# Kernel tuning notes

Measured on AMD Instinct MI355X. Metric: run time of the kernel, lower is better.

## Reference

```python
import jax, jax.numpy as jnp
import numpy as np

MIN_, MAX_, KSZ, IGNORE_IDX = 10, 10, 3, -255
B, H, W = 256, 256, 256
LI_MAX_ITERS = 64


def setup_inputs() -> dict:
    key = jax.random.key(0)
    x = jax.random.uniform(key, (B, 1, H, W), dtype=jnp.float32)
    return {"x": x}


def _otsu(hist):
    # hist: [256] counts. Returns Otsu threshold (bin value); fg = img > t.
    bins = jnp.arange(256, dtype=jnp.float32)
    w0 = jnp.cumsum(hist)[:-1]
    w1 = hist.sum() - w0
    s0 = jnp.cumsum(hist * bins)[:-1]
    s_tot = (hist * bins).sum()
    m0 = s0 / jnp.maximum(w0, 1e-12)
    m1 = (s_tot - s0) / jnp.maximum(w1, 1e-12)
    var_b = w0 * w1 * (m0 - m1) ** 2
    return jnp.argmax(var_b).astype(jnp.float32)


def _li(hist, init_t):
    # Histogram-based Li iterative minimum cross-entropy threshold
    # (skimage.filters.threshold_li with initial_guess=init_t).
    bins = jnp.arange(256, dtype=jnp.float32)
    img_min = jnp.min(jnp.where(hist > 0, bins, 255.0))
    vals = bins - img_min  # shift so values >= 0 (as skimage does)
    csum = jnp.cumsum(hist)
    cvsum = jnp.cumsum(hist * vals)
    n_tot, s_tot = csum[-1], cvsum[-1]
    tol = 0.5  # integer image -> half the minimal value spacing

    def body(state):
        t_curr, _, i = state
        # background: img <= t_curr + img_min
        idx = jnp.clip(jnp.floor(t_curr + img_min).astype(jnp.int32), 0, 255)
        n_back, s_back = csum[idx], cvsum[idx]
        n_fore, s_fore = n_tot - n_back, s_tot - s_back
        mean_back = jnp.where(n_back > 0, s_back / jnp.maximum(n_back, 1.0), 0.0)
        mean_fore = s_fore / jnp.maximum(n_fore, 1.0)
        eps = 1e-12
        t_next = (mean_back - mean_fore) / (
            jnp.log(jnp.maximum(mean_back, eps)) - jnp.log(jnp.maximum(mean_fore, eps)))
        t_next = jnp.where(mean_back < eps, mean_fore / 2.0, t_next)
        return (t_next, t_curr, i + 1)

    def cond(state):
        t_curr, t_prev, i = state
        return (jnp.abs(t_curr - t_prev) > tol) & (i < LI_MAX_ITERS)

    t0 = init_t - img_min
    t_fin, _, _ = jax.lax.while_loop(cond, body, (t0, t0 + 10.0, 0))
    return t_fin + img_min


def _sample_mask(key, region, k):
    # Uniform sampling without replacement of up to k pixels from region
    # (bool [H,W]) via random-score top-k (equiv. to torch.multinomial
    # with uniform probs, w/o replacement).
    flat = region.reshape(-1)
    scores = jnp.where(flat, jax.random.uniform(key, (flat.shape[0],)), -1.0)
    top, idx = jax.lax.top_k(scores, k)
    valid = (top >= 0.0).astype(jnp.int32)
    mask = jnp.zeros(flat.shape[0], jnp.int32).at[idx].max(valid)
    return mask.reshape(region.shape)


def _dilate(m):
    # kornia dilation with ones (KSZ,KSZ) kernel on a 0/1 mask == max filter.
    return jax.lax.reduce_window(m, 0, jax.lax.max, (KSZ, KSZ), (1, 1), "SAME")


def _per_image(img_u8, key_fg, key_bg):
    # img_u8: [H,W] int32 in [0,255]
    hist = jnp.zeros(256, jnp.float32).at[img_u8.ravel()].add(1.0)
    otsu = jnp.clip(_otsu(hist), 1.0, 254.0)  # clamp 0->1, 255->254
    li_t = _li(hist, otsu)
    roi = img_u8.astype(jnp.float32) > li_t

    fg = _sample_mask(key_fg, roi, MAX_)
    bg = _sample_mask(key_bg, jnp.logical_not(roi), MIN_)
    if KSZ > 1:
        fg = _dilate(fg)
        bg = _dilate(bg)

    overlap = (fg + bg) == 2
    fg = jnp.where(overlap, 0, fg)
    bg = jnp.where(overlap, 0, bg)

    seeds = jnp.full((H, W), IGNORE_IDX, jnp.int32)
    seeds = jnp.where(bg == 1, 0, seeds)
    seeds = jnp.where(fg == 1, 1, seeds)
    return seeds


def reference(x):
    b = x.shape[0]
    # (cam*255).astype(uint8): truncation, cam in [0,1]
    img = jnp.clip(jnp.floor(x[:, 0] * 255.0), 0, 255).astype(jnp.int32)
    keys = jax.random.split(jax.random.key(1), (b, 2))
    return jax.vmap(_per_image)(img, keys[:, 0], keys[:, 1])
```

## Files before the change

kernel.cpp:

```cpp
#include <hip/hip_runtime.h>
#include <stdint.h>

#define NPIX 65536
#define IGN (-255)
#define CAP 768
#define LCAP 192
#define HPART  16384
#define M_CF   18432
#define M_CB   18433
#define M_THR  18434
#define M_NROI 18435
#define M_FG   18436
#define M_BG   19204
#define SCR_I4 5120

__device__ __forceinline__ uint32_t rotl32(uint32_t v, uint32_t r){ return (v<<r)|(v>>(32u-r)); }

__device__ __forceinline__ void tf2x32(uint32_t k0, uint32_t k1, uint32_t x0, uint32_t x1,
                                       uint32_t &o0, uint32_t &o1){
  uint32_t k2 = k0 ^ k1 ^ 0x1BD11BDAu;
  x0 += k0; x1 += k1;
#define TFR(r) { x0 += x1; x1 = rotl32(x1,(r)); x1 ^= x0; }
  TFR(13u) TFR(15u) TFR(26u) TFR(6u)   x0 += k1; x1 += k2 + 1u;
  TFR(17u) TFR(29u) TFR(16u) TFR(24u)  x0 += k2; x1 += k0 + 2u;
  TFR(13u) TFR(15u) TFR(26u) TFR(6u)   x0 += k0; x1 += k1 + 3u;
  TFR(17u) TFR(29u) TFR(16u) TFR(24u)  x0 += k1; x1 += k2 + 4u;
  TFR(13u) TFR(15u) TFR(26u) TFR(6u)   x0 += k2; x1 += k0 + 5u;
#undef TFR
  o0 = x0; o1 = x1;
}

__device__ __forceinline__ unsigned long long packCand(uint32_t bits, uint32_t pix){
  float f = __uint_as_float((bits >> 9) | 0x3f800000u) - 1.0f;
  uint32_t u = __float_as_uint(f) ^ 0x80000000u;
  return ((unsigned long long)u << 32) | (unsigned long long)(0xFFFFFFFFu - pix);
}

__device__ __forceinline__ void t10_insert(unsigned long long* l, unsigned long long c){
  if (c > l[9]) {
    l[9] = c;
#pragma unroll
    for (int i = 9; i > 0; --i){
      unsigned long long a = l[i-1], b2 = l[i];
      if (b2 > a){ l[i-1] = b2; l[i] = a; }
    }
  }
}

__global__ __launch_bounds__(256, 8)
void k1_hist_fill(const float* __restrict__ x, int* __restrict__ out){
  const int blk = blockIdx.x;
  const int b = blk >> 3, j8 = blk & 7;
  const int tid = threadIdx.x;
  const float4* x4 = (const float4*)(x + (size_t)b * NPIX);
  int* base = out + (size_t)b * NPIX;
  int4* o4 = (int4*)base;

  __shared__ uint32_t histR[1024];
#pragma unroll
  for (int k = 0; k < 4; ++k) histR[tid + 256*k] = 0u;
  if (j8 == 0 && tid == 0){ base[M_CF] = 0; base[M_CB] = 0; }
  __syncthreads();

  const int4 f4 = make_int4(IGN, IGN, IGN, IGN);
  const uint32_t c4 = (uint32_t)(tid & 3);
#pragma unroll
  for (int jj = 0; jj < 8; ++jj){
    int i4 = j8*2048 + jj*256 + tid;
    float4 v = x4[i4];
    uint32_t u0 = (uint32_t)min(max((int)floorf(v.x*255.0f),0),255);
    uint32_t u1 = (uint32_t)min(max((int)floorf(v.y*255.0f),0),255);
    uint32_t u2 = (uint32_t)min(max((int)floorf(v.z*255.0f),0),255);
    uint32_t u3 = (uint32_t)min(max((int)floorf(v.w*255.0f),0),255);
    base[i4] = (int)(u0 | (u1<<8) | (u2<<16) | (u3<<24));
    if (i4 >= SCR_I4) o4[i4] = f4;
    atomicAdd(&histR[(u0<<2)|c4],1u); atomicAdd(&histR[(u1<<2)|c4],1u);
    atomicAdd(&histR[(u2<<2)|c4],1u); atomicAdd(&histR[(u3<<2)|c4],1u);
  }
  __syncthreads();
  uint32_t s = histR[4*tid] + histR[4*tid+1] + histR[4*tid+2] + histR[4*tid+3];
  base[HPART + j8*256 + tid] = (int)s;
}

__global__ __launch_bounds__(256, 8)
void k2_score(int* __restrict__ out){
  const int blk = blockIdx.x;
  const int b = blk >> 3, j8 = blk & 7;
  const int tid = threadIdx.x;
  int* meta = out + (size_t)b * NPIX;

  __shared__ float csum[256], cvsum[256];
  __shared__ int s_imin, s_qthr;
  __shared__ unsigned long long s_best;
  __shared__ uint32_t s_kw[4];
  __shared__ int s_lcnt[2], s_base[2];
  __shared__ int s_lbuf[2][LCAP];

  if (tid == 0){ s_imin = 255; s_best = 0ull; s_lcnt[0] = 0; s_lcnt[1] = 0; }
  if (tid < 2){
    uint32_t o0, o1;
    tf2x32(0u, 1u, 0u, (uint32_t)(2*b + tid), o0, o1);
    s_kw[2*tid] = o0; s_kw[2*tid+1] = o1;
  }
  __syncthreads();

  int h = 0;
#pragma unroll
  for (int j = 0; j < 8; ++j) h += meta[HPART + j*256 + tid];
  if (h) atomicMin(&s_imin, tid);
  __syncthreads();
  const float img_min = (float)s_imin;

  csum[tid]  = (float)h;
  cvsum[tid] = (float)h * ((float)tid - img_min);
  __syncthreads();
  for (int off = 1; off < 256; off <<= 1){
    float a = 0.f, c2 = 0.f;
    if (tid >= off){ a = csum[tid-off]; c2 = cvsum[tid-off]; }
    __syncthreads();
    if (tid >= off){ csum[tid] += a; cvsum[tid] += c2; }
    __syncthreads();
  }
  {
    float s_tot_o = cvsum[255] + img_min * csum[255];
    if (tid < 255){
      float w0 = csum[tid];
      float w1 = 65536.0f - w0;
      float cs = cvsum[tid] + img_min * csum[tid];
      float m0 = cs / fmaxf(w0, 1e-12f);
      float m1 = (s_tot_o - cs) / fmaxf(w1, 1e-12f);
      float d = m0 - m1;
      float vb = (w0*w1) * (d*d);
      unsigned long long pk =
        ((unsigned long long)__float_as_uint(vb) << 32) | (unsigned long long)(255 - tid);
      atomicMax(&s_best, pk);
    }
  }
  __syncthreads();
  if (tid == 0){
    int bestIdx = 255 - (int)(s_best & 0xFFFFFFFFull);
    float otsu = fminf(fmaxf((float)bestIdx, 1.0f), 254.0f);
    float n_tot = csum[255], s_tot = cvsum[255];
    float t_curr = otsu - img_min, t_prev = t_curr + 10.0f;
    int it = 0;
    while (fabsf(t_curr - t_prev) > 0.5f && it < 64){
      int idx = min(max((int)floorf(t_curr + img_min), 0), 255);
      float n_back = csum[idx], s_back = cvsum[idx];
      float n_fore = n_tot - n_back, s_fore = s_tot - s_back;
      float mean_back = (n_back > 0.0f) ? (s_back / fmaxf(n_back, 1.0f)) : 0.0f;
      float mean_fore = s_fore / fmaxf(n_fore, 1.0f);
      float t_next = (mean_back - mean_fore) /
                     (logf(fmaxf(mean_back, 1e-12f)) - logf(fmaxf(mean_fore, 1e-12f)));
      if (mean_back < 1e-12f) t_next = mean_fore * 0.5f;
      t_prev = t_curr; t_curr = t_next; ++it;
    }
    float lit = t_curr + img_min;
    int qthr;
    if (!(lit == lit)) qthr = 256;
    else               qthr = (int)floorf(lit) + 1;
    s_qthr = qthr;
    if (j8 == 0){
      meta[M_THR] = qthr;
      int nlo = (qthr <= 0) ? 0 : (int)csum[min(qthr, 256) - 1];
      meta[M_NROI] = NPIX - nlo;
    }
  }
  __syncthreads();

  const int qthr = s_qthr;
  const uint32_t fk0 = s_kw[0], fk1 = s_kw[1], bk0 = s_kw[2], bk1 = s_kw[3];
  const int4* u4 = (const int4*)meta;
  int4 w0 = u4[j8*512 + tid];
  int4 w1 = u4[j8*512 + 256 + tid];
  const uint32_t pixA = (uint32_t)(j8*8192 + 16*tid);
  const uint32_t pixB = pixA + 4096u;
#pragma unroll
  for (int half = 0; half < 2; ++half){
    int4 w = half ? w1 : w0;
    uint32_t pb = half ? pixB : pixA;
    const uint32_t words[4] = {(uint32_t)w.x,(uint32_t)w.y,(uint32_t)w.z,(uint32_t)w.w};
#pragma unroll
    for (int m = 0; m < 4; ++m){
      uint32_t pk = words[m];
#pragma unroll
      for (int s = 0; s < 4; ++s){
        int q = (int)((pk >> (8*s)) & 255u);
        bool r = (q >= qthr);
        uint32_t pix = pb + (uint32_t)(4*m + s);
        uint32_t o0, o1;
        tf2x32(r ? fk0 : bk0, r ? fk1 : bk1, 0u, pix, o0, o1);
        uint32_t bits = o0 ^ o1;
        if (bits >= 0xFF000000u){
          int r2 = r ? 0 : 1;
          int idx = atomicAdd(&s_lcnt[r2], 1);
          if (idx < LCAP) s_lbuf[r2][idx] = (int)pix;
        }
      }
    }
  }
  __syncthreads();
  if (tid < 2){
    int n = s_lcnt[tid];
    int add = (n > LCAP) ? (n + CAP + 1) : n;
    s_base[tid] = atomicAdd(&meta[M_CF + tid], add);
  }
  __syncthreads();
#pragma unroll
  for (int r2 = 0; r2 < 2; ++r2){
    int n = min(s_lcnt[r2], LCAP);
    int bse = s_base[r2];
    for (int i = tid; i < n; i += 256){
      int g = bse + i;
      if (g < CAP) meta[(r2 ? M_BG : M_FG) + g] = s_lbuf[r2][i];
    }
  }
}

__global__ __launch_bounds__(256, 4)
void k3_final(int* __restrict__ out){
  const int b = blockIdx.x;
  const int tid = threadIdx.x;
  int* meta = out + (size_t)b * NPIX;
  int* outb = meta;

  __shared__ unsigned long long s_top[2][64][10];
  __shared__ unsigned long long s_top2[2][8][10];
  __shared__ uint32_t s_kw[4];
  __shared__ int s_cnt[2], s_fail[2], s_np[2];
  __shared__ int s_qthr;
  __shared__ int s_pr[2][10], s_pc[2][10];

  if (tid < 2){
    uint32_t o0, o1;
    tf2x32(0u, 1u, 0u, (uint32_t)(2*b + tid), o0, o1);
    s_kw[2*tid] = o0; s_kw[2*tid+1] = o1;
  }
  if (tid == 0){
    s_qthr = meta[M_THR];
    int nroi = meta[M_NROI];
    int c0 = meta[M_CF], c1 = meta[M_CB];
    s_cnt[0] = c0; s_cnt[1] = c1;
    s_fail[0] = (c0 > CAP) || (c0 < 10 && c0 != nroi);
    s_fail[1] = (c1 > CAP) || (c1 < 10 && c1 != NPIX - nroi);
  }
  __syncthreads();

  const int wv = tid >> 6, lane = tid & 63;
  if (wv < 2){
    const int r2 = wv;
    unsigned long long t[10];
#pragma unroll
    for (int i = 0; i < 10; ++i) t[i] = 0ull;
    const uint32_t kk0 = s_kw[2*r2], kk1 = s_kw[2*r2+1];
    if (!s_fail[r2]){
      int n = min(s_cnt[r2], CAP);
      for (int i = lane; i < n; i += 64){
        uint32_t pix = (uint32_t)meta[(r2 ? M_BG : M_FG) + i];
        uint32_t o0, o1; tf2x32(kk0, kk1, 0u, pix, o0, o1);
        t10_insert(t, packCand(o0 ^ o1, pix));
      }
    } else {
      const int qthr = s_qthr;
      for (int k = 0; k < 1024; ++k){
        uint32_t pix = (uint32_t)(lane + 64*k);
        int q = (int)(((uint32_t)meta[pix >> 2] >> (8*(pix & 3u))) & 255u);
        bool r = (q >= qthr);
        if (r == (r2 == 0)){
          uint32_t o0, o1; tf2x32(kk0, kk1, 0u, pix, o0, o1);
          t10_insert(t, packCand(o0 ^ o1, pix));
        }
      }
    }
#pragma unroll
    for (int i = 0; i < 10; ++i) s_top[r2][lane][i] = t[i];
  }
  __syncthreads();
  if (wv < 2 && lane < 8){
    unsigned long long t[10];
#pragma unroll
    for (int i = 0; i < 10; ++i) t[i] = 0ull;
    for (int l2 = 0; l2 < 8; ++l2)
#pragma unroll
      for (int i = 0; i < 10; ++i) t10_insert(t, s_top[wv][lane*8 + l2][i]);
#pragma unroll
    for (int i = 0; i < 10; ++i) s_top2[wv][lane][i] = t[i];
  }
  __syncthreads();
  if (wv < 2 && lane == 0){
    unsigned long long t[10];
#pragma unroll
    for (int i = 0; i < 10; ++i) t[i] = 0ull;
    for (int l2 = 0; l2 < 8; ++l2)
#pragma unroll
      for (int i = 0; i < 10; ++i) t10_insert(t, s_top2[wv][l2][i]);
    int np = 0;
    for (int i = 0; i < 10; ++i){
      if (t[i]){
        uint32_t pix = 0xFFFFFFFFu - (uint32_t)(t[i] & 0xFFFFFFFFull);
        s_pr[wv][np] = (int)(pix >> 8);
        s_pc[wv][np] = (int)(pix & 255u);
        ++np;
      }
    }
    s_np[wv] = np;
  }
  __syncthreads();

  const int4 f4 = make_int4(IGN, IGN, IGN, IGN);
#pragma unroll
  for (int k = 0; k < 20; ++k)
    ((int4*)meta)[tid + 256*k] = f4;
  __syncthreads();

  const int nfg = s_np[0], nbg = s_np[1];
  const int npts = nfg + nbg;
  if (tid < npts*9){
    int k = tid / 9, d = tid - k*9;
    int pr = (k < nfg) ? s_pr[0][k] : s_pr[1][k - nfg];
    int pc = (k < nfg) ? s_pc[0][k] : s_pc[1][k - nfg];
    pr += d/3 - 1; pc += d%3 - 1;
    if (pr >= 0 && pr < 256 && pc >= 0 && pc < 256){
      bool fgd = false, bgd = false;
      for (int i = 0; i < nfg; ++i) fgd |= (abs(pr - s_pr[0][i]) <= 1) && (abs(pc - s_pc[0][i]) <= 1);
      for (int i = 0; i < nbg; ++i) bgd |= (abs(pr - s_pr[1][i]) <= 1) && (abs(pc - s_pc[1][i]) <= 1);
      int val = (fgd && bgd) ? IGN : (fgd ? 1 : 0);
      outb[pr*256 + pc] = val;
    }
  }
}

extern "C" void kernel_launch(void* const* d_in, const int* in_sizes, int n_in,
                              void* d_out, int out_size, void* d_ws, size_t ws_size,
                              hipStream_t stream) {
  const float* x = (const float*)d_in[0];
  int* out = (int*)d_out;
  int B = in_sizes[0] / NPIX;
  k1_hist_fill<<<8*B, 256, 0, stream>>>(x, out);
  k2_score    <<<8*B, 256, 0, stream>>>(out);
  k3_final    <<<B,   256, 0, stream>>>(out);
}
```

Measured before the change: 200.8 us.

## Prefilter random candidates for both classes in histogram pass, merge scoring into final kernel

The first kernel now runs the Threefry hash for every pixel under both the foreground and background keys while it builds the histogram. It records high-score candidates per segment, so the thresholded pixel scan of the old second kernel goes away and the packed-u8 image store is no longer needed. The final kernel computes Otsu/Li itself, re-reads the original floats only for the candidates, and builds the top-k from shared memory. This saves one launch and one full-image pass at the cost of doubling hash work in k1 and making k2 do the threshold work with only B blocks.

```diff
diff --git a/kernel.cpp b/kernel.cpp
--- a/kernel.cpp
+++ b/kernel.cpp
@@ -3,16 +3,14 @@
 
 #define NPIX 65536
 #define IGN (-255)
-#define CAP 768
-#define LCAP 192
-#define HPART  16384
-#define M_CF   18432
-#define M_CB   18433
-#define M_THR  18434
-#define M_NROI 18435
-#define M_FG   18436
-#define M_BG   19204
-#define SCR_I4 5120
+#define SEGC 96
+#define GCAP 768
+#define FGSEG 0
+#define BGSEG 768
+#define CNTF  1536
+#define CNTB  1544
+#define HPART 1552
+#define SCRI4 1024
 
 __device__ __forceinline__ uint32_t rotl32(uint32_t v, uint32_t r){ return (v<<r)|(v>>(32u-r)); }
 
@@ -48,20 +46,28 @@
 }
 
 __global__ __launch_bounds__(256, 8)
-void k1_hist_fill(const float* __restrict__ x, int* __restrict__ out){
+void k1_main(const float* __restrict__ x, int* __restrict__ out){
   const int blk = blockIdx.x;
   const int b = blk >> 3, j8 = blk & 7;
   const int tid = threadIdx.x;
   const float4* x4 = (const float4*)(x + (size_t)b * NPIX);
-  int* base = out + (size_t)b * NPIX;
-  int4* o4 = (int4*)base;
+  int* meta = out + (size_t)b * NPIX;
+  int4* o4 = (int4*)meta;
 
   __shared__ uint32_t histR[1024];
+  __shared__ uint32_t s_kw[4];
+  __shared__ int s_lcnt[2];
 #pragma unroll
   for (int k = 0; k < 4; ++k) histR[tid + 256*k] = 0u;
-  if (j8 == 0 && tid == 0){ base[M_CF] = 0; base[M_CB] = 0; }
-  __syncthreads();
-
+  if (tid < 2){
+    uint32_t o0, o1;
+    tf2x32(0u, 1u, 0u, (uint32_t)(2*b + tid), o0, o1);
+    s_kw[2*tid] = o0; s_kw[2*tid+1] = o1;
+    s_lcnt[tid] = 0;
+  }
+  __syncthreads();
+
+  const uint32_t fk0 = s_kw[0], fk1 = s_kw[1], bk0 = s_kw[2], bk1 = s_kw[3];
   const int4 f4 = make_int4(IGN, IGN, IGN, IGN);
   const uint32_t c4 = (uint32_t)(tid & 3);
 #pragma unroll
@@ -72,35 +78,56 @@
     uint32_t u1 = (uint32_t)min(max((int)floorf(v.y*255.0f),0),255);
     uint32_t u2 = (uint32_t)min(max((int)floorf(v.z*255.0f),0),255);
     uint32_t u3 = (uint32_t)min(max((int)floorf(v.w*255.0f),0),255);
-    base[i4] = (int)(u0 | (u1<<8) | (u2<<16) | (u3<<24));
-    if (i4 >= SCR_I4) o4[i4] = f4;
     atomicAdd(&histR[(u0<<2)|c4],1u); atomicAdd(&histR[(u1<<2)|c4],1u);
     atomicAdd(&histR[(u2<<2)|c4],1u); atomicAdd(&histR[(u3<<2)|c4],1u);
+    if (i4 >= SCRI4) o4[i4] = f4;
+    uint32_t pix0 = (uint32_t)(4*i4);
+#pragma unroll
+    for (int s = 0; s < 4; ++s){
+      uint32_t pix = pix0 + (uint32_t)s;
+      uint32_t a0, a1, c0, c1;
+      tf2x32(fk0, fk1, 0u, pix, a0, a1);
+      tf2x32(bk0, bk1, 0u, pix, c0, c1);
+      if ((a0 ^ a1) >= 0xFF000000u){
+        int idx = atomicAdd(&s_lcnt[0], 1);
+        if (idx < SEGC) meta[FGSEG + j8*SEGC + idx] = (int)pix;
+      }
+      if ((c0 ^ c1) >= 0xFF000000u){
+        int idx = atomicAdd(&s_lcnt[1], 1);
+        if (idx < SEGC) meta[BGSEG + j8*SEGC + idx] = (int)pix;
+      }
+    }
   }
   __syncthreads();
   uint32_t s = histR[4*tid] + histR[4*tid+1] + histR[4*tid+2] + histR[4*tid+3];
-  base[HPART + j8*256 + tid] = (int)s;
-}
-
-__global__ __launch_bounds__(256, 8)
-void k2_score(int* __restrict__ out){
-  const int blk = blockIdx.x;
-  const int b = blk >> 3, j8 = blk & 7;
+  meta[HPART + j8*256 + tid] = (int)s;
+  if (tid < 2) meta[(tid ? CNTB : CNTF) + j8] = s_lcnt[tid];
+}
+
+__global__ __launch_bounds__(256, 2)
+void k2_final(const float* __restrict__ x, int* __restrict__ out){
+  const int b = blockIdx.x;
   const int tid = threadIdx.x;
   int* meta = out + (size_t)b * NPIX;
+  int* outb = meta;
+  const float* img = x + (size_t)b * NPIX;
 
   __shared__ float csum[256], cvsum[256];
-  __shared__ int s_imin, s_qthr;
+  __shared__ int s_imin, s_qthr, s_nroi;
   __shared__ unsigned long long s_best;
   __shared__ uint32_t s_kw[4];
-  __shared__ int s_lcnt[2], s_base[2];
-  __shared__ int s_lbuf[2][LCAP];
-
-  if (tid == 0){ s_imin = 255; s_best = 0ull; s_lcnt[0] = 0; s_lcnt[1] = 0; }
+  __shared__ int s_cand[2][GCAP];
+  __shared__ int s_cc[2], s_ovf[2], s_fail[2], s_np[2];
+  __shared__ unsigned long long s_top[2][64][10];
+  __shared__ unsigned long long s_top2[2][8][10];
+  __shared__ int s_pr[2][10], s_pc[2][10];
+
+  if (tid == 0){ s_imin = 255; s_best = 0ull; }
   if (tid < 2){
     uint32_t o0, o1;
     tf2x32(0u, 1u, 0u, (uint32_t)(2*b + tid), o0, o1);
     s_kw[2*tid] = o0; s_kw[2*tid+1] = o1;
+    s_cc[tid] = 0;
   }
   __syncthreads();
 
@@ -121,6 +148,7 @@
     if (tid >= off){ csum[tid] += a; cvsum[tid] += c2; }
     __syncthreads();
   }
+
   {
     float s_tot_o = cvsum[255] + img_min * csum[255];
     if (tid < 255){
@@ -137,6 +165,7 @@
     }
   }
   __syncthreads();
+
   if (tid == 0){
     int bestIdx = 255 - (int)(s_best & 0xFFFFFFFFull);
     float otsu = fminf(fmaxf((float)bestIdx, 1.0f), 254.0f);
@@ -159,89 +188,43 @@
     if (!(lit == lit)) qthr = 256;
     else               qthr = (int)floorf(lit) + 1;
     s_qthr = qthr;
-    if (j8 == 0){
-      meta[M_THR] = qthr;
-      int nlo = (qthr <= 0) ? 0 : (int)csum[min(qthr, 256) - 1];
-      meta[M_NROI] = NPIX - nlo;
-    }
+    int nlo = (qthr <= 0) ? 0 : (int)csum[min(qthr, 256) - 1];
+    s_nroi = NPIX - nlo;
+  }
+  if (tid < 2){
+    int gc = 0, ovf = 0;
+#pragma unroll
+    for (int j = 0; j < 8; ++j){
+      int c = meta[(tid ? CNTB : CNTF) + j];
+      gc += c; if (c > SEGC) ovf = 1;
+    }
+    s_ovf[tid] = ovf | (gc > GCAP);
   }
   __syncthreads();
 
   const int qthr = s_qthr;
-  const uint32_t fk0 = s_kw[0], fk1 = s_kw[1], bk0 = s_kw[2], bk1 = s_kw[3];
-  const int4* u4 = (const int4*)meta;
-  int4 w0 = u4[j8*512 + tid];
-  int4 w1 = u4[j8*512 + 256 + tid];
-  const uint32_t pixA = (uint32_t)(j8*8192 + 16*tid);
-  const uint32_t pixB = pixA + 4096u;
-#pragma unroll
-  for (int half = 0; half < 2; ++half){
-    int4 w = half ? w1 : w0;
-    uint32_t pb = half ? pixB : pixA;
-    const uint32_t words[4] = {(uint32_t)w.x,(uint32_t)w.y,(uint32_t)w.z,(uint32_t)w.w};
-#pragma unroll
-    for (int m = 0; m < 4; ++m){
-      uint32_t pk = words[m];
-#pragma unroll
-      for (int s = 0; s < 4; ++s){
-        int q = (int)((pk >> (8*s)) & 255u);
-        bool r = (q >= qthr);
-        uint32_t pix = pb + (uint32_t)(4*m + s);
-        uint32_t o0, o1;
-        tf2x32(r ? fk0 : bk0, r ? fk1 : bk1, 0u, pix, o0, o1);
-        uint32_t bits = o0 ^ o1;
-        if (bits >= 0xFF000000u){
-          int r2 = r ? 0 : 1;
-          int idx = atomicAdd(&s_lcnt[r2], 1);
-          if (idx < LCAP) s_lbuf[r2][idx] = (int)pix;
+#pragma unroll
+  for (int r2 = 0; r2 < 2; ++r2){
+    for (int i = tid; i < GCAP; i += 256){
+      int j = i / SEGC, k = i - j*SEGC;
+      int cnt = min(meta[(r2 ? CNTB : CNTF) + j], SEGC);
+      if (k < cnt){
+        uint32_t pix = (uint32_t)meta[(r2 ? BGSEG : FGSEG) + i];
+        float v = img[pix];
+        int q = min(max((int)floorf(v*255.0f),0),255);
+        bool roi = (q >= qthr);
+        if (roi == (r2 == 0)){
+          int idx = atomicAdd(&s_cc[r2], 1);
+          s_cand[r2][idx] = (int)pix;
         }
       }
     }
   }
   __syncthreads();
   if (tid < 2){
-    int n = s_lcnt[tid];
-    int add = (n > LCAP) ? (n + CAP + 1) : n;
-    s_base[tid] = atomicAdd(&meta[M_CF + tid], add);
-  }
-  __syncthreads();
-#pragma unroll
-  for (int r2 = 0; r2 < 2; ++r2){
-    int n = min(s_lcnt[r2], LCAP);
-    int bse = s_base[r2];
-    for (int i = tid; i < n; i += 256){
-      int g = bse + i;
-      if (g < CAP) meta[(r2 ? M_BG : M_FG) + g] = s_lbuf[r2][i];
-    }
-  }
-}
-
-__global__ __launch_bounds__(256, 4)
-void k3_final(int* __restrict__ out){
-  const int b = blockIdx.x;
-  const int tid = threadIdx.x;
-  int* meta = out + (size_t)b * NPIX;
-  int* outb = meta;
-
-  __shared__ unsigned long long s_top[2][64][10];
-  __shared__ unsigned long long s_top2[2][8][10];
-  __shared__ uint32_t s_kw[4];
-  __shared__ int s_cnt[2], s_fail[2], s_np[2];
-  __shared__ int s_qthr;
-  __shared__ int s_pr[2][10], s_pc[2][10];
-
-  if (tid < 2){
-    uint32_t o0, o1;
-    tf2x32(0u, 1u, 0u, (uint32_t)(2*b + tid), o0, o1);
-    s_kw[2*tid] = o0; s_kw[2*tid+1] = o1;
-  }
-  if (tid == 0){
-    s_qthr = meta[M_THR];
-    int nroi = meta[M_NROI];
-    int c0 = meta[M_CF], c1 = meta[M_CB];
-    s_cnt[0] = c0; s_cnt[1] = c1;
-    s_fail[0] = (c0 > CAP) || (c0 < 10 && c0 != nroi);
-    s_fail[1] = (c1 > CAP) || (c1 < 10 && c1 != NPIX - nroi);
+    int rs = tid ? (NPIX - s_nroi) : s_nroi;
+    int cc = s_cc[tid];
+    s_fail[tid] = s_ovf[tid] || (cc < 10 && cc != rs);
   }
   __syncthreads();
 
@@ -253,19 +236,19 @@
     for (int i = 0; i < 10; ++i) t[i] = 0ull;
     const uint32_t kk0 = s_kw[2*r2], kk1 = s_kw[2*r2+1];
     if (!s_fail[r2]){
-      int n = min(s_cnt[r2], CAP);
+      int n = s_cc[r2];
       for (int i = lane; i < n; i += 64){
-        uint32_t pix = (uint32_t)meta[(r2 ? M_BG : M_FG) + i];
+        uint32_t pix = (uint32_t)s_cand[r2][i];
         uint32_t o0, o1; tf2x32(kk0, kk1, 0u, pix, o0, o1);
         t10_insert(t, packCand(o0 ^ o1, pix));
       }
     } else {
-      const int qthr = s_qthr;
       for (int k = 0; k < 1024; ++k){
         uint32_t pix = (uint32_t)(lane + 64*k);
-        int q = (int)(((uint32_t)meta[pix >> 2] >> (8*(pix & 3u))) & 255u);
-        bool r = (q >= qthr);
-        if (r == (r2 == 0)){
+        float v = img[pix];
+        int q = min(max((int)floorf(v*255.0f),0),255);
+        bool roi = (q >= qthr);
+        if (roi == (r2 == 0)){
           uint32_t o0, o1; tf2x32(kk0, kk1, 0u, pix, o0, o1);
           t10_insert(t, packCand(o0 ^ o1, pix));
         }
@@ -308,7 +291,7 @@
 
   const int4 f4 = make_int4(IGN, IGN, IGN, IGN);
 #pragma unroll
-  for (int k = 0; k < 20; ++k)
+  for (int k = 0; k < 4; ++k)
     ((int4*)meta)[tid + 256*k] = f4;
   __syncthreads();
 
@@ -335,7 +318,6 @@
   const float* x = (const float*)d_in[0];
   int* out = (int*)d_out;
   int B = in_sizes[0] / NPIX;
-  k1_hist_fill<<<8*B, 256, 0, stream>>>(x, out);
-  k2_score    <<<8*B, 256, 0, stream>>>(out);
-  k3_final    <<<B,   256, 0, stream>>>(out);
-}
+  k1_main <<<8*B, 256, 0, stream>>>(x, out);
+  k2_final<<<B,   256, 0, stream>>>(x, out);
+}
```

Measured after the change: 191.6 us. 1.05x faster.

## Fuse scoring and final selection into one 1024-thread per-image kernel

Applied to the files above, without the earlier changes.

Merges the per-slice scoring kernel and the final top-k/dilation kernel into a single kernel with one 1024-thread block per image. Candidates are kept as packed keys in shared memory, so the global atomics, the metadata round trip and the Threefry recomputation in the final stage go away. Otsu and Li thresholds are now computed once per image rather than eight times. The cost is less parallelism: 256 large blocks instead of 2048 small ones, plus a larger shared-memory footprint that may limit occupancy.

```diff
diff --git a/kernel.cpp b/kernel.cpp
--- a/kernel.cpp
+++ b/kernel.cpp
@@ -4,15 +4,8 @@
 #define NPIX 65536
 #define IGN (-255)
 #define CAP 768
-#define LCAP 192
-#define HPART  16384
-#define M_CF   18432
-#define M_CB   18433
-#define M_THR  18434
-#define M_NROI 18435
-#define M_FG   18436
-#define M_BG   19204
-#define SCR_I4 5120
+#define HPART 16384
+#define SCRI4 4608
 
 __device__ __forceinline__ uint32_t rotl32(uint32_t v, uint32_t r){ return (v<<r)|(v>>(32u-r)); }
 
@@ -48,7 +41,7 @@
 }
 
 __global__ __launch_bounds__(256, 8)
-void k1_hist_fill(const float* __restrict__ x, int* __restrict__ out){
+void k1_stream(const float* __restrict__ x, int* __restrict__ out){
   const int blk = blockIdx.x;
   const int b = blk >> 3, j8 = blk & 7;
   const int tid = threadIdx.x;
@@ -59,7 +52,6 @@
   __shared__ uint32_t histR[1024];
 #pragma unroll
   for (int k = 0; k < 4; ++k) histR[tid + 256*k] = 0u;
-  if (j8 == 0 && tid == 0){ base[M_CF] = 0; base[M_CB] = 0; }
   __syncthreads();
 
   const int4 f4 = make_int4(IGN, IGN, IGN, IGN);
@@ -73,7 +65,7 @@
     uint32_t u2 = (uint32_t)min(max((int)floorf(v.z*255.0f),0),255);
     uint32_t u3 = (uint32_t)min(max((int)floorf(v.w*255.0f),0),255);
     base[i4] = (int)(u0 | (u1<<8) | (u2<<16) | (u3<<24));
-    if (i4 >= SCR_I4) o4[i4] = f4;
+    if (i4 >= SCRI4) o4[i4] = f4;
     atomicAdd(&histR[(u0<<2)|c4],1u); atomicAdd(&histR[(u1<<2)|c4],1u);
     atomicAdd(&histR[(u2<<2)|c4],1u); atomicAdd(&histR[(u3<<2)|c4],1u);
   }
@@ -82,45 +74,53 @@
   base[HPART + j8*256 + tid] = (int)s;
 }
 
-__global__ __launch_bounds__(256, 8)
-void k2_score(int* __restrict__ out){
-  const int blk = blockIdx.x;
-  const int b = blk >> 3, j8 = blk & 7;
+__global__ __launch_bounds__(1024, 4)
+void k2_final(int* __restrict__ out){
+  const int b = blockIdx.x;
   const int tid = threadIdx.x;
   int* meta = out + (size_t)b * NPIX;
+  int* outb = meta;
 
   __shared__ float csum[256], cvsum[256];
-  __shared__ int s_imin, s_qthr;
+  __shared__ int s_imin, s_qthr, s_nroi;
   __shared__ unsigned long long s_best;
   __shared__ uint32_t s_kw[4];
-  __shared__ int s_lcnt[2], s_base[2];
-  __shared__ int s_lbuf[2][LCAP];
-
-  if (tid == 0){ s_imin = 255; s_best = 0ull; s_lcnt[0] = 0; s_lcnt[1] = 0; }
+  __shared__ unsigned long long buf[2][CAP];
+  __shared__ int s_cnt[2], s_fail[2], s_np[2];
+  __shared__ unsigned long long s_top[2][64][10];
+  __shared__ unsigned long long s_top2[2][8][10];
+  __shared__ int s_pr[2][10], s_pc[2][10];
+
+  if (tid == 0){ s_imin = 255; s_best = 0ull; }
   if (tid < 2){
     uint32_t o0, o1;
     tf2x32(0u, 1u, 0u, (uint32_t)(2*b + tid), o0, o1);
     s_kw[2*tid] = o0; s_kw[2*tid+1] = o1;
+    s_cnt[tid] = 0;
   }
   __syncthreads();
 
   int h = 0;
-#pragma unroll
-  for (int j = 0; j < 8; ++j) h += meta[HPART + j*256 + tid];
-  if (h) atomicMin(&s_imin, tid);
+  if (tid < 256){
+#pragma unroll
+    for (int j = 0; j < 8; ++j) h += meta[HPART + j*256 + tid];
+    if (h) atomicMin(&s_imin, tid);
+  }
   __syncthreads();
   const float img_min = (float)s_imin;
-
-  csum[tid]  = (float)h;
-  cvsum[tid] = (float)h * ((float)tid - img_min);
+  if (tid < 256){
+    csum[tid]  = (float)h;
+    cvsum[tid] = (float)h * ((float)tid - img_min);
+  }
   __syncthreads();
   for (int off = 1; off < 256; off <<= 1){
     float a = 0.f, c2 = 0.f;
-    if (tid >= off){ a = csum[tid-off]; c2 = cvsum[tid-off]; }
+    if (tid < 256 && tid >= off){ a = csum[tid-off]; c2 = cvsum[tid-off]; }
     __syncthreads();
-    if (tid >= off){ csum[tid] += a; cvsum[tid] += c2; }
+    if (tid < 256 && tid >= off){ csum[tid] += a; cvsum[tid] += c2; }
     __syncthreads();
   }
+
   {
     float s_tot_o = cvsum[255] + img_min * csum[255];
     if (tid < 255){
@@ -137,6 +137,7 @@
     }
   }
   __syncthreads();
+
   if (tid == 0){
     int bestIdx = 255 - (int)(s_best & 0xFFFFFFFFull);
     float otsu = fminf(fmaxf((float)bestIdx, 1.0f), 254.0f);
@@ -159,25 +160,19 @@
     if (!(lit == lit)) qthr = 256;
     else               qthr = (int)floorf(lit) + 1;
     s_qthr = qthr;
-    if (j8 == 0){
-      meta[M_THR] = qthr;
-      int nlo = (qthr <= 0) ? 0 : (int)csum[min(qthr, 256) - 1];
-      meta[M_NROI] = NPIX - nlo;
-    }
+    int nlo = (qthr <= 0) ? 0 : (int)csum[min(qthr, 256) - 1];
+    s_nroi = NPIX - nlo;
   }
   __syncthreads();
 
   const int qthr = s_qthr;
   const uint32_t fk0 = s_kw[0], fk1 = s_kw[1], bk0 = s_kw[2], bk1 = s_kw[3];
   const int4* u4 = (const int4*)meta;
-  int4 w0 = u4[j8*512 + tid];
-  int4 w1 = u4[j8*512 + 256 + tid];
-  const uint32_t pixA = (uint32_t)(j8*8192 + 16*tid);
-  const uint32_t pixB = pixA + 4096u;
-#pragma unroll
-  for (int half = 0; half < 2; ++half){
-    int4 w = half ? w1 : w0;
-    uint32_t pb = half ? pixB : pixA;
+  int4 w0 = u4[tid], w1 = u4[tid + 1024], w2 = u4[tid + 2048], w3 = u4[tid + 3072];
+#pragma unroll
+  for (int k = 0; k < 4; ++k){
+    int4 w = (k == 0) ? w0 : (k == 1) ? w1 : (k == 2) ? w2 : w3;
+    uint32_t pb = (uint32_t)(16*(tid + 1024*k));
     const uint32_t words[4] = {(uint32_t)w.x,(uint32_t)w.y,(uint32_t)w.z,(uint32_t)w.w};
 #pragma unroll
     for (int m = 0; m < 4; ++m){
@@ -192,56 +187,18 @@
         uint32_t bits = o0 ^ o1;
         if (bits >= 0xFF000000u){
           int r2 = r ? 0 : 1;
-          int idx = atomicAdd(&s_lcnt[r2], 1);
-          if (idx < LCAP) s_lbuf[r2][idx] = (int)pix;
+          int idx = atomicAdd(&s_cnt[r2], 1);
+          if (idx < CAP) buf[r2][idx] = packCand(bits, pix);
         }
       }
     }
   }
   __syncthreads();
+
   if (tid < 2){
-    int n = s_lcnt[tid];
-    int add = (n > LCAP) ? (n + CAP + 1) : n;
-    s_base[tid] = atomicAdd(&meta[M_CF + tid], add);
-  }
-  __syncthreads();
-#pragma unroll
-  for (int r2 = 0; r2 < 2; ++r2){
-    int n = min(s_lcnt[r2], LCAP);
-    int bse = s_base[r2];
-    for (int i = tid; i < n; i += 256){
-      int g = bse + i;
-      if (g < CAP) meta[(r2 ? M_BG : M_FG) + g] = s_lbuf[r2][i];
-    }
-  }
-}
-
-__global__ __launch_bounds__(256, 4)
-void k3_final(int* __restrict__ out){
-  const int b = blockIdx.x;
-  const int tid = threadIdx.x;
-  int* meta = out + (size_t)b * NPIX;
-  int* outb = meta;
-
-  __shared__ unsigned long long s_top[2][64][10];
-  __shared__ unsigned long long s_top2[2][8][10];
-  __shared__ uint32_t s_kw[4];
-  __shared__ int s_cnt[2], s_fail[2], s_np[2];
-  __shared__ int s_qthr;
-  __shared__ int s_pr[2][10], s_pc[2][10];
-
-  if (tid < 2){
-    uint32_t o0, o1;
-    tf2x32(0u, 1u, 0u, (uint32_t)(2*b + tid), o0, o1);
-    s_kw[2*tid] = o0; s_kw[2*tid+1] = o1;
-  }
-  if (tid == 0){
-    s_qthr = meta[M_THR];
-    int nroi = meta[M_NROI];
-    int c0 = meta[M_CF], c1 = meta[M_CB];
-    s_cnt[0] = c0; s_cnt[1] = c1;
-    s_fail[0] = (c0 > CAP) || (c0 < 10 && c0 != nroi);
-    s_fail[1] = (c1 > CAP) || (c1 < 10 && c1 != NPIX - nroi);
+    int rs = tid ? (NPIX - s_nroi) : s_nroi;
+    int cc = s_cnt[tid];
+    s_fail[tid] = (cc > CAP) || (cc < 10 && cc != rs);
   }
   __syncthreads();
 
@@ -251,16 +208,11 @@
     unsigned long long t[10];
 #pragma unroll
     for (int i = 0; i < 10; ++i) t[i] = 0ull;
-    const uint32_t kk0 = s_kw[2*r2], kk1 = s_kw[2*r2+1];
     if (!s_fail[r2]){
       int n = min(s_cnt[r2], CAP);
-      for (int i = lane; i < n; i += 64){
-        uint32_t pix = (uint32_t)meta[(r2 ? M_BG : M_FG) + i];
-        uint32_t o0, o1; tf2x32(kk0, kk1, 0u, pix, o0, o1);
-        t10_insert(t, packCand(o0 ^ o1, pix));
-      }
+      for (int i = lane; i < n; i += 64) t10_insert(t, buf[r2][i]);
     } else {
-      const int qthr = s_qthr;
+      const uint32_t kk0 = s_kw[2*r2], kk1 = s_kw[2*r2+1];
       for (int k = 0; k < 1024; ++k){
         uint32_t pix = (uint32_t)(lane + 64*k);
         int q = (int)(((uint32_t)meta[pix >> 2] >> (8*(pix & 3u))) & 255u);
@@ -308,8 +260,10 @@
 
   const int4 f4 = make_int4(IGN, IGN, IGN, IGN);
 #pragma unroll
-  for (int k = 0; k < 20; ++k)
-    ((int4*)meta)[tid + 256*k] = f4;
+  for (int k = 0; k < 5; ++k){
+    int idx = tid + 1024*k;
+    if (idx < SCRI4) ((int4*)meta)[idx] = f4;
+  }
   __syncthreads();
 
   const int nfg = s_np[0], nbg = s_np[1];
@@ -335,7 +289,6 @@
   const float* x = (const float*)d_in[0];
   int* out = (int*)d_out;
   int B = in_sizes[0] / NPIX;
-  k1_hist_fill<<<8*B, 256, 0, stream>>>(x, out);
-  k2_score    <<<8*B, 256, 0, stream>>>(out);
-  k3_final    <<<B,   256, 0, stream>>>(out);
-}
+  k1_stream<<<8*B, 256, 0, stream>>>(x, out);
+  k2_final <<<B,  1024, 0, stream>>>(out);
+}
```

After: 184.1 us. 8.3% less time.
